# Kernel optimization log

Hardware: AMD Instinct MI355X
Metric: run time of the kernel (lower is better)

Reference implementation:

```python
import jax, jax.numpy as jnp
import numpy as np

SIZE = (4096, 4096)   # self.size
SIGMA = 1.0           # blur_sigma
NOISE_STD = 0.01      # noise_std


def _gauss_kernel(sigma):
    # scipy.ndimage.gaussian_filter: radius = int(truncate*sigma + 0.5), truncate=4.0
    r = int(4.0 * sigma + 0.5)
    x = np.arange(-r, r + 1, dtype=np.float32)
    k = np.exp(-0.5 * (x / sigma) ** 2)
    k = k / k.sum()
    return jnp.asarray(k), r


def _blur(img, sigma):
    # img: [C, H, W]; separable Gaussian, scipy mode='reflect' == jnp symmetric pad
    k, r = _gauss_kernel(sigma)
    x = jnp.pad(img, ((0, 0), (r, r), (r, r)), mode='symmetric')
    x = x[:, None]  # [C, 1, H+2r, W+2r] (NCHW)
    kh = k.reshape(1, 1, -1, 1)
    kw = k.reshape(1, 1, 1, -1)
    x = jax.lax.conv_general_dilated(x, kh, (1, 1), 'VALID')
    x = jax.lax.conv_general_dilated(x, kw, (1, 1), 'VALID')
    return x[:, 0]  # [C, H, W]


def setup_inputs() -> dict:
    key = jax.random.key(0)
    k1, k2 = jax.random.split(key)
    img = jax.random.normal(k1, (1, 2048, 2048), dtype=jnp.float32)
    noise = jax.random.normal(k2, (1,) + SIZE, dtype=jnp.float32)
    return {"img": img, "noise": noise}


def reference(img, noise):
    # bilinear resize, align_corners=False == jax half-pixel linear resize
    img = jax.image.resize(img, (img.shape[0],) + SIZE, method='linear')
    img = jnp.flip(img, axis=2)   # horizontal flip
    img = jnp.flip(img, axis=1)   # vertical flip
    img = jnp.rot90(img, k=1, axes=(1, 2))  # rot90, k fixed to 1
    img = img + noise * NOISE_STD
    img = _blur(img, SIGMA)
    img = jnp.log1p(jnp.clip(img, 0.0))  # clamp(min=0) then log1p
    return img
```

## Files before the change

### kernel.cpp

```cpp
#include <hip/hip_runtime.h>
#include <math.h>

#define N      4096
#define NIMG   2048
#define TXO    56
#define HR     40
#define DRS    48
#define IPP    27
#define IPR    34
#define VB     64
#define NSX    74
#define NSY    103
#define NSTRIP (NSX * NSY)
#define NBLK   ((NSTRIP + 3) / 4)

#define KW0 0.00013383063f
#define KW1 0.00443186160f
#define KW2 0.05399112800f
#define KW3 0.24197144000f
#define KW4 0.39894346870f

__device__ __forceinline__ int symi(int g) {
    g = (g < 0) ? (-1 - g) : g;
    g = (g >= N) ? (2 * N - 1 - g) : g;
    return g;
}

__global__ __launch_bounds__(256, 5)
void TensorAugment_79216376807666_kernel(const float* __restrict__ img,
                                         const float* __restrict__ noise,
                                         float* __restrict__ out) {
    __shared__ float SH[4 * (IPR * IPP + 8 * VB)];

    const int tid  = threadIdx.x;
    const int lane = tid & 63;
    const int wave = tid >> 6;

    float* const IP   = SH + wave * (IPR * IPP + 8 * VB);
    float* const VBUF = IP + IPR * IPP;

    const int strip0 = blockIdx.x * 4 + wave;
    if (strip0 >= NSTRIP) return;

    const int strip = __builtin_amdgcn_readfirstlane(strip0);
    const int sx = strip % NSX;
    const int sy = strip / NSX;
    const int x0 = sx * TXO;
    const int y0 = sy * HR;

    int gxa = x0 - 4, gxb = x0 + 59;
    int mxa = symi(gxa), mxb = symi(gxb);
    int gxmin = min(mxa, mxb), gxmax = max(mxa, mxb);
    if (gxa <= 0) gxmin = 0;
    if (gxb >= N - 1) gxmax = N - 1;
    int umin = (N - 1) - gxmax, umax = (N - 1) - gxmin;
    int r0min = (umin - 1) >> 1;
    int r0max = (umax - 1) >> 1;
    int nrows = r0max - r0min + 2;

    int gya = y0 - 4, gyb = y0 + DRS - 5;
    int mya = symi(gya), myb = symi(gyb);
    int gymin = min(mya, myb), gymax = max(mya, myb);
    if (gya <= 0) gymin = 0;
    if (gyb >= N - 1) gymax = N - 1;
    int c0min = (gymin - 1) >> 1;
    int c0max = (gymax - 1) >> 1;
    int ncols = c0max - c0min + 2;

    {
        const int c  = lane & 31;
        const int rb = lane >> 5;
        const bool cok = (c < ncols);
#pragma unroll
        for (int k = 0; k < 17; ++k) {
            const int r = rb + 2 * k;
            if (cok && r < nrows) {
                const int ir = min(max(r0min + r, 0), NIMG - 1);
                const int ic = min(max(c0min + c, 0), NIMG - 1);
                IP[r * IPP + c] = img[ir * NIMG + ic];
            }
        }
    }

    const int gx  = x0 - 4 + lane;
    const int gxm = symi(gx);
    const int u   = (N - 1) - gxm;
    const int r0  = (u - 1) >> 1;
    const float wr1 = (u & 1) ? 0.25f : 0.75f;
    const float wr0 = 1.0f - wr1;
    const int a0  = (r0 - r0min) * IPP;
    const bool oklane = (lane >= 4) && (lane < 60) && (gx < N);
    const int rbase = min(max(lane - 4, 0), VB - 9);

    const float kk[9] = {KW0, KW1, KW2, KW3, KW4, KW3, KW2, KW1, KW0};

    auto nzld = [&](int dr) -> float {
        const int gym = symi(y0 - 4 + dr);
        return noise[(size_t)gym * N + gxm];
    };
    auto drow = [&](int dr, float nz) -> float {
        const int gym = symi(y0 - 4 + dr);
        const int jc  = ((gym - 1) >> 1) - c0min;
        const float wc1 = (gym & 1) ? 0.25f : 0.75f;
        const float wc0 = 1.0f - wc1;
        const float f0 = IP[a0 + jc],       f1 = IP[a0 + jc + 1];
        const float f2 = IP[a0 + IPP + jc], f3 = IP[a0 + IPP + jc + 1];
        const float top = fmaf(wc0, f0, wc1 * f1);
        const float bot = fmaf(wc0, f2, wc1 * f3);
        return fmaf(0.01f, nz, fmaf(wr0, top, wr1 * bot));
    };

    float win[16];
    {
        float nz[16];
#pragma unroll
        for (int j = 0; j < 16; ++j) nz[j] = nzld(j);
#pragma unroll
        for (int j = 0; j < 16; ++j) win[j] = drow(j, nz[j]);
    }

#pragma unroll 1
    for (int ck = 2; ck <= 6; ++ck) {
        float nz[8];
        if (ck < 6) {
#pragma unroll
            for (int j = 0; j < 8; ++j) nz[j] = nzld(8 * ck + j);
        }

#pragma unroll
        for (int j = 0; j < 8; ++j) {
            float acc = kk[0] * win[j];
#pragma unroll
            for (int i = 1; i < 9; ++i) acc = fmaf(kk[i], win[j + i], acc);
            VBUF[j * VB + lane] = acc;
        }

        const int gyb0 = y0 + 8 * (ck - 2);
#pragma unroll
        for (int j = 0; j < 8; ++j) {
            const int vb = j * VB + rbase;
            float acc = kk[0] * VBUF[vb];
#pragma unroll
            for (int i = 1; i < 9; ++i) acc = fmaf(kk[i], VBUF[vb + i], acc);
            acc = fmaxf(acc, 0.0f);
            const float r = __logf(1.0f + acc);
            const int gy = gyb0 + j;
            if (oklane && gy < N) out[(size_t)gy * N + gx] = r;
        }

        if (ck < 6) {
#pragma unroll
            for (int i = 0; i < 8; ++i) win[i] = win[i + 8];
#pragma unroll
            for (int j = 0; j < 8; ++j) win[8 + j] = drow(8 * ck + j, nz[j]);
        }
    }
}

extern "C" void kernel_launch(void* const* d_in, const int* in_sizes, int n_in,
                              void* d_out, int out_size, void* d_ws, size_t ws_size,
                              hipStream_t stream) {
    const float* img   = (const float*)d_in[0];
    const float* noise = (const float*)d_in[1];
    float* out = (float*)d_out;

    dim3 grid(NBLK);
    TensorAugment_79216376807666_kernel<<<grid, 256, 0, stream>>>(img, noise, out);
}
```

Measured before the change: 149.0 us.

## Replace LDS horizontal blur with ds_bpermute and specialize interior strip upsampling

The horizontal 9-tap pass now exchanges neighbour values across lanes with ds_bpermute instead of writing to and reading back from a shared-memory buffer, which removes the VBUF allocation. The smaller LDS footprint lets launch bounds rise to 6 waves per SIMD. Interior strips also get a fast path that reuses six row-interpolated values to produce eight output rows and loads noise with plain strided addressing instead of per-row reflect arithmetic. The cost is more code, the risk of register pressure under the tighter launch bound, and bpermute latency, which is still LDS-bound.

```diff
diff --git a/kernel.cpp b/kernel.cpp
--- a/kernel.cpp
+++ b/kernel.cpp
@@ -8,7 +8,6 @@
 #define DRS    48
 #define IPP    27
 #define IPR    34
-#define VB     64
 #define NSX    74
 #define NSY    103
 #define NSTRIP (NSX * NSY)
@@ -26,18 +25,54 @@
     return g;
 }
 
-__global__ __launch_bounds__(256, 5)
+
+#define PRODUCE8(M, OFS, NZA, NOFS)                                            \
+    do {                                                                       \
+        if (yin) {                                                             \
+            const int ab_ = a0 + 4 * (M);                                      \
+            float g0 = fmaf(wr0, IP[ab_ + 0], wr1 * IP[ab_ + IPP + 0]);        \
+            float g1 = fmaf(wr0, IP[ab_ + 1], wr1 * IP[ab_ + IPP + 1]);        \
+            float g2 = fmaf(wr0, IP[ab_ + 2], wr1 * IP[ab_ + IPP + 2]);        \
+            float g3 = fmaf(wr0, IP[ab_ + 3], wr1 * IP[ab_ + IPP + 3]);        \
+            float g4 = fmaf(wr0, IP[ab_ + 4], wr1 * IP[ab_ + IPP + 4]);        \
+            float g5 = fmaf(wr0, IP[ab_ + 5], wr1 * IP[ab_ + IPP + 5]);        \
+            win[(OFS) + 0] = fmaf(0.25f, g0, fmaf(0.75f, g1, 0.01f * (NZA)[(NOFS) + 0])); \
+            win[(OFS) + 1] = fmaf(0.75f, g1, fmaf(0.25f, g2, 0.01f * (NZA)[(NOFS) + 1])); \
+            win[(OFS) + 2] = fmaf(0.25f, g1, fmaf(0.75f, g2, 0.01f * (NZA)[(NOFS) + 2])); \
+            win[(OFS) + 3] = fmaf(0.75f, g2, fmaf(0.25f, g3, 0.01f * (NZA)[(NOFS) + 3])); \
+            win[(OFS) + 4] = fmaf(0.25f, g2, fmaf(0.75f, g3, 0.01f * (NZA)[(NOFS) + 4])); \
+            win[(OFS) + 5] = fmaf(0.75f, g3, fmaf(0.25f, g4, 0.01f * (NZA)[(NOFS) + 5])); \
+            win[(OFS) + 6] = fmaf(0.25f, g3, fmaf(0.75f, g4, 0.01f * (NZA)[(NOFS) + 6])); \
+            win[(OFS) + 7] = fmaf(0.75f, g4, fmaf(0.25f, g5, 0.01f * (NZA)[(NOFS) + 7])); \
+        } else {                                                               \
+            _Pragma("unroll")                                                  \
+            for (int j_ = 0; j_ < 8; ++j_) {                                   \
+                const int dr_  = 8 * (M) + j_;                                 \
+                const int gym_ = symi(y0 - 4 + dr_);                           \
+                const int jc_  = ((gym_ - 1) >> 1) - c0min;                    \
+                const float wc1_ = (gym_ & 1) ? 0.25f : 0.75f;                 \
+                const float wc0_ = 1.0f - wc1_;                                \
+                const float f0_ = IP[a0 + jc_],       f1_ = IP[a0 + jc_ + 1];  \
+                const float f2_ = IP[a0 + IPP + jc_], f3_ = IP[a0 + IPP + jc_ + 1]; \
+                const float top_ = fmaf(wc0_, f0_, wc1_ * f1_);                \
+                const float bot_ = fmaf(wc0_, f2_, wc1_ * f3_);                \
+                win[(OFS) + j_] = fmaf(0.01f, (NZA)[(NOFS) + j_],              \
+                                       fmaf(wr0, top_, wr1 * bot_));           \
+            }                                                                  \
+        }                                                                      \
+    } while (0)
+
+__global__ __launch_bounds__(256, 6)
 void TensorAugment_79216376807666_kernel(const float* __restrict__ img,
                                          const float* __restrict__ noise,
                                          float* __restrict__ out) {
-    __shared__ float SH[4 * (IPR * IPP + 8 * VB)];
+    __shared__ float SH[4 * IPR * IPP];
 
     const int tid  = threadIdx.x;
     const int lane = tid & 63;
     const int wave = tid >> 6;
 
-    float* const IP   = SH + wave * (IPR * IPP + 8 * VB);
-    float* const VBUF = IP + IPR * IPP;
+    float* const IP = SH + wave * (IPR * IPP);
 
     const int strip0 = blockIdx.x * 4 + wave;
     if (strip0 >= NSTRIP) return;
@@ -47,6 +82,7 @@
     const int sy = strip / NSX;
     const int x0 = sx * TXO;
     const int y0 = sy * HR;
+    const bool yin = (sy > 0) && (sy < NSY - 1);
 
     int gxa = x0 - 4, gxb = x0 + 59;
     int mxa = symi(gxa), mxb = symi(gxb);
@@ -90,58 +126,65 @@
     const float wr0 = 1.0f - wr1;
     const int a0  = (r0 - r0min) * IPP;
     const bool oklane = (lane >= 4) && (lane < 60) && (gx < N);
-    const int rbase = min(max(lane - 4, 0), VB - 9);
-
-    const float kk[9] = {KW0, KW1, KW2, KW3, KW4, KW3, KW2, KW1, KW0};
-
-    auto nzld = [&](int dr) -> float {
-        const int gym = symi(y0 - 4 + dr);
-        return noise[(size_t)gym * N + gxm];
-    };
-    auto drow = [&](int dr, float nz) -> float {
-        const int gym = symi(y0 - 4 + dr);
-        const int jc  = ((gym - 1) >> 1) - c0min;
-        const float wc1 = (gym & 1) ? 0.25f : 0.75f;
-        const float wc0 = 1.0f - wc1;
-        const float f0 = IP[a0 + jc],       f1 = IP[a0 + jc + 1];
-        const float f2 = IP[a0 + IPP + jc], f3 = IP[a0 + IPP + jc + 1];
-        const float top = fmaf(wc0, f0, wc1 * f1);
-        const float bot = fmaf(wc0, f2, wc1 * f3);
-        return fmaf(0.01f, nz, fmaf(wr0, top, wr1 * bot));
-    };
+
+    int ba[9];
+#pragma unroll
+    for (int d = 0; d < 9; ++d) ba[d] = 4 * (lane + d - 4);
+
+    const float* const nzb = noise + ((size_t)max(y0 - 4, 0) * N + gxm);
 
     float win[16];
     {
-        float nz[16];
-#pragma unroll
-        for (int j = 0; j < 16; ++j) nz[j] = nzld(j);
-#pragma unroll
-        for (int j = 0; j < 16; ++j) win[j] = drow(j, nz[j]);
+        float nzp[16];
+        if (yin) {
+#pragma unroll
+            for (int j = 0; j < 16; ++j) nzp[j] = nzb[(size_t)j * N];
+        } else {
+#pragma unroll
+            for (int j = 0; j < 16; ++j)
+                nzp[j] = noise[(size_t)symi(y0 - 4 + j) * N + gxm];
+        }
+        PRODUCE8(0, 0, nzp, 0);
+        PRODUCE8(1, 8, nzp, 8);
     }
 
 #pragma unroll 1
     for (int ck = 2; ck <= 6; ++ck) {
-        float nz[8];
+        float nz8[8];
         if (ck < 6) {
-#pragma unroll
-            for (int j = 0; j < 8; ++j) nz[j] = nzld(8 * ck + j);
-        }
-
+            if (yin) {
+                const float* nr = nzb + (size_t)(8 * ck) * N;
+#pragma unroll
+                for (int j = 0; j < 8; ++j) nz8[j] = nr[(size_t)j * N];
+            } else {
+#pragma unroll
+                for (int j = 0; j < 8; ++j)
+                    nz8[j] = noise[(size_t)symi(y0 - 4 + 8 * ck + j) * N + gxm];
+            }
+        }
+
+        const int gyb0 = y0 + 8 * (ck - 2);
 #pragma unroll
         for (int j = 0; j < 8; ++j) {
-            float acc = kk[0] * win[j];
-#pragma unroll
-            for (int i = 1; i < 9; ++i) acc = fmaf(kk[i], win[j + i], acc);
-            VBUF[j * VB + lane] = acc;
-        }
-
-        const int gyb0 = y0 + 8 * (ck - 2);
-#pragma unroll
-        for (int j = 0; j < 8; ++j) {
-            const int vb = j * VB + rbase;
-            float acc = kk[0] * VBUF[vb];
-#pragma unroll
-            for (int i = 1; i < 9; ++i) acc = fmaf(kk[i], VBUF[vb + i], acc);
+            float v = KW0 * win[j];
+            v = fmaf(KW1, win[j + 1], v);
+            v = fmaf(KW2, win[j + 2], v);
+            v = fmaf(KW3, win[j + 3], v);
+            v = fmaf(KW4, win[j + 4], v);
+            v = fmaf(KW3, win[j + 5], v);
+            v = fmaf(KW2, win[j + 6], v);
+            v = fmaf(KW1, win[j + 7], v);
+            v = fmaf(KW0, win[j + 8], v);
+            const int vi = __float_as_int(v);
+            float acc = KW4 * v;
+            acc = fmaf(KW0, __int_as_float(__builtin_amdgcn_ds_bpermute(ba[0], vi)), acc);
+            acc = fmaf(KW1, __int_as_float(__builtin_amdgcn_ds_bpermute(ba[1], vi)), acc);
+            acc = fmaf(KW2, __int_as_float(__builtin_amdgcn_ds_bpermute(ba[2], vi)), acc);
+            acc = fmaf(KW3, __int_as_float(__builtin_amdgcn_ds_bpermute(ba[3], vi)), acc);
+            acc = fmaf(KW3, __int_as_float(__builtin_amdgcn_ds_bpermute(ba[5], vi)), acc);
+            acc = fmaf(KW2, __int_as_float(__builtin_amdgcn_ds_bpermute(ba[6], vi)), acc);
+            acc = fmaf(KW1, __int_as_float(__builtin_amdgcn_ds_bpermute(ba[7], vi)), acc);
+            acc = fmaf(KW0, __int_as_float(__builtin_amdgcn_ds_bpermute(ba[8], vi)), acc);
             acc = fmaxf(acc, 0.0f);
             const float r = __logf(1.0f + acc);
             const int gy = gyb0 + j;
@@ -151,8 +194,7 @@
         if (ck < 6) {
 #pragma unroll
             for (int i = 0; i < 8; ++i) win[i] = win[i + 8];
-#pragma unroll
-            for (int j = 0; j < 8; ++j) win[8 + j] = drow(8 * ck + j, nz[j]);
+            PRODUCE8(ck, 8, nz8, 0);
         }
     }
 }
```

New measurement: 145.9 us. -2.1%, faster.

## Widen strips to 4 columns per lane with float4 I/O and interior fast path

Applied to the files above, without the earlier changes.

Each wave now covers a 256-wide by 16-row strip, with every lane producing 4 adjacent output columns through float4 noise loads and float4 stores. Interior strips take a specialized path that computes the bilinear upsample with fixed 0.25/0.75 weights and no reflection index math, while border strips keep a general path. The horizontal pass exchanges neighbor quads through a small double-buffered LDS slot instead of a 64-wide row buffer. The aim is less scalar memory traffic, less index arithmetic and less halo overhead. In exchange it uses more registers per thread, lowers the occupancy hint from 5 to 4, and spends more of each strip on vertical halo rows.

```diff
diff --git a/kernel.cpp b/kernel.cpp
--- a/kernel.cpp
+++ b/kernel.cpp
@@ -3,14 +3,16 @@
 
 #define N      4096
 #define NIMG   2048
-#define TXO    56
-#define HR     40
-#define DRS    48
-#define IPP    27
-#define IPR    34
-#define VB     64
-#define NSX    74
-#define NSY    103
+#define SPAN   256
+#define TXN    248
+#define HR     16
+#define DRS    24
+#define IPP    15
+#define IPR    130
+#define IPOFF  1952
+#define WSZ    (IPOFF + 512)
+#define NSX    17
+#define NSY    256
 #define NSTRIP (NSX * NSY)
 #define NBLK   ((NSTRIP + 3) / 4)
 
@@ -26,18 +28,82 @@
     return g;
 }
 
-__global__ __launch_bounds__(256, 5)
+#define H9(A,B,C,D,E,F,G,H,I)                                                  \
+    fmaf(KW0,(A), fmaf(KW1,(B), fmaf(KW2,(C), fmaf(KW3,(D), fmaf(KW4,(E),     \
+    fmaf(KW3,(F), fmaf(KW2,(G), fmaf(KW1,(H), KW0*(I)))))))))
+
+#define GCOL(J, G) do {                                                        \
+    const float p0_ = IP[ipb - 2*IPP + (J)];                                   \
+    const float p1_ = IP[ipb -   IPP + (J)];                                   \
+    const float p2_ = IP[ipb         + (J)];                                   \
+    const float p3_ = IP[ipb +   IPP + (J)];                                   \
+    (G).x = fmaf(0.75f, p2_, 0.25f * p3_);                                     \
+    (G).y = fmaf(0.25f, p1_, 0.75f * p2_);                                     \
+    (G).z = fmaf(0.75f, p1_, 0.25f * p2_);                                     \
+    (G).w = fmaf(0.25f, p0_, 0.75f * p1_);                                     \
+} while (0)
+
+#define DMIX(DST, W0, GA_, W1, GB_, NZ) do {                                   \
+    (DST).x = fmaf(W0, (GA_).x, fmaf(W1, (GB_).x, 0.01f * (NZ).x));            \
+    (DST).y = fmaf(W0, (GA_).y, fmaf(W1, (GB_).y, 0.01f * (NZ).y));            \
+    (DST).z = fmaf(W0, (GA_).z, fmaf(W1, (GB_).z, 0.01f * (NZ).z));            \
+    (DST).w = fmaf(W0, (GA_).w, fmaf(W1, (GB_).w, 0.01f * (NZ).w));            \
+} while (0)
+
+#define PROD4F(JN, W0_, W1_, W2_, W3_, Z0, Z1, Z2, Z3) do {                    \
+    float4 gc_, gd_;                                                           \
+    GCOL((JN), gc_);  GCOL((JN) + 1, gd_);                                     \
+    DMIX(W0_, 0.25f, ga, 0.75f, gb,  Z0);                                      \
+    DMIX(W1_, 0.75f, gb, 0.25f, gc_, Z1);                                      \
+    DMIX(W2_, 0.25f, gb, 0.75f, gc_, Z2);                                      \
+    DMIX(W3_, 0.75f, gc_, 0.25f, gd_, Z3);                                     \
+    ga = gc_;  gb = gd_;                                                       \
+} while (0)
+
+#define OUT1(K, GY) do {                                                       \
+    float4 v_;                                                                 \
+    v_.x = H9(win[K].x, win[K+1].x, win[K+2].x, win[K+3].x, win[K+4].x,        \
+              win[K+5].x, win[K+6].x, win[K+7].x, win[K+8].x);                 \
+    v_.y = H9(win[K].y, win[K+1].y, win[K+2].y, win[K+3].y, win[K+4].y,        \
+              win[K+5].y, win[K+6].y, win[K+7].y, win[K+8].y);                 \
+    v_.z = H9(win[K].z, win[K+1].z, win[K+2].z, win[K+3].z, win[K+4].z,        \
+              win[K+5].z, win[K+6].z, win[K+7].z, win[K+8].z);                 \
+    v_.w = H9(win[K].w, win[K+1].w, win[K+2].w, win[K+3].w, win[K+4].w,        \
+              win[K+5].w, win[K+6].w, win[K+7].w, win[K+8].w);                 \
+    float* vx_ = ((K) & 1) ? VX1 : VX0;                                        \
+    *reinterpret_cast<float4*>(vx_ + 4 * lane) = v_;                           \
+    const float4 wl_ = *reinterpret_cast<const float4*>(vx_ + 4 * lnL);        \
+    const float4 wr_ = *reinterpret_cast<const float4*>(vx_ + 4 * lnR);        \
+    float4 r_;                                                                 \
+    r_.x = H9(wl_.x, wl_.y, wl_.z, wl_.w, v_.x, v_.y, v_.z, v_.w, wr_.x);      \
+    r_.y = H9(wl_.y, wl_.z, wl_.w, v_.x, v_.y, v_.z, v_.w, wr_.x, wr_.y);      \
+    r_.z = H9(wl_.z, wl_.w, v_.x, v_.y, v_.z, v_.w, wr_.x, wr_.y, wr_.z);      \
+    r_.w = H9(wl_.w, v_.x, v_.y, v_.z, v_.w, wr_.x, wr_.y, wr_.z, wr_.w);      \
+    r_.x = __logf(1.0f + fmaxf(r_.x, 0.0f));                                   \
+    r_.y = __logf(1.0f + fmaxf(r_.y, 0.0f));                                   \
+    r_.z = __logf(1.0f + fmaxf(r_.z, 0.0f));                                   \
+    r_.w = __logf(1.0f + fmaxf(r_.w, 0.0f));                                   \
+    if (okst) *reinterpret_cast<float4*>(out + (size_t)(GY) * N + gxs) = r_;   \
+} while (0)
+
+#define SLIDE4() do {                                                          \
+    _Pragma("unroll")                                                          \
+    for (int i_ = 0; i_ < 8; ++i_) win[i_] = win[i_ + 4];                      \
+} while (0)
+
+__global__ __launch_bounds__(256, 4)
 void TensorAugment_79216376807666_kernel(const float* __restrict__ img,
                                          const float* __restrict__ noise,
                                          float* __restrict__ out) {
-    __shared__ float SH[4 * (IPR * IPP + 8 * VB)];
+    __shared__ __align__(16) float SH[4 * WSZ];
 
     const int tid  = threadIdx.x;
     const int lane = tid & 63;
     const int wave = tid >> 6;
 
-    float* const IP   = SH + wave * (IPR * IPP + 8 * VB);
-    float* const VBUF = IP + IPR * IPP;
+    float* const IP  = SH + wave * WSZ;
+    float* const VX0 = IP + IPOFF;
+    float* const VX1 = VX0 + 256;
 
     const int strip0 = blockIdx.x * 4 + wave;
     if (strip0 >= NSTRIP) return;
@@ -45,10 +111,12 @@
     const int strip = __builtin_amdgcn_readfirstlane(strip0);
     const int sx = strip % NSX;
     const int sy = strip / NSX;
-    const int x0 = sx * TXO;
+    const int x0 = sx * TXN;
     const int y0 = sy * HR;
-
-    int gxa = x0 - 4, gxb = x0 + 59;
+    const bool xin = (sx > 0) && (sx < NSX - 1);
+    const bool yin = (sy > 0) && (sy < NSY - 1);
+
+    int gxa = x0 - 4, gxb = x0 + SPAN - 5;
     int mxa = symi(gxa), mxb = symi(gxb);
     int gxmin = min(mxa, mxb), gxmax = max(mxa, mxb);
     if (gxa <= 0) gxmin = 0;
@@ -68,12 +136,12 @@
     int ncols = c0max - c0min + 2;
 
     {
-        const int c  = lane & 31;
-        const int rb = lane >> 5;
+        const int c  = lane & 15;
+        const int rb = lane >> 4;
         const bool cok = (c < ncols);
 #pragma unroll
-        for (int k = 0; k < 17; ++k) {
-            const int r = rb + 2 * k;
+        for (int k = 0; k < 33; ++k) {
+            const int r = rb + 4 * k;
             if (cok && r < nrows) {
                 const int ir = min(max(r0min + r, 0), NIMG - 1);
                 const int ic = min(max(c0min + c, 0), NIMG - 1);
@@ -82,77 +150,117 @@
         }
     }
 
-    const int gx  = x0 - 4 + lane;
-    const int gxm = symi(gx);
-    const int u   = (N - 1) - gxm;
-    const int r0  = (u - 1) >> 1;
-    const float wr1 = (u & 1) ? 0.25f : 0.75f;
-    const float wr0 = 1.0f - wr1;
-    const int a0  = (r0 - r0min) * IPP;
-    const bool oklane = (lane >= 4) && (lane < 60) && (gx < N);
-    const int rbase = min(max(lane - 4, 0), VB - 9);
-
-    const float kk[9] = {KW0, KW1, KW2, KW3, KW4, KW3, KW2, KW1, KW0};
-
-    auto nzld = [&](int dr) -> float {
-        const int gym = symi(y0 - 4 + dr);
-        return noise[(size_t)gym * N + gxm];
-    };
-    auto drow = [&](int dr, float nz) -> float {
-        const int gym = symi(y0 - 4 + dr);
-        const int jc  = ((gym - 1) >> 1) - c0min;
-        const float wc1 = (gym & 1) ? 0.25f : 0.75f;
-        const float wc0 = 1.0f - wc1;
-        const float f0 = IP[a0 + jc],       f1 = IP[a0 + jc + 1];
-        const float f2 = IP[a0 + IPP + jc], f3 = IP[a0 + IPP + jc + 1];
-        const float top = fmaf(wc0, f0, wc1 * f1);
-        const float bot = fmaf(wc0, f2, wc1 * f3);
-        return fmaf(0.01f, nz, fmaf(wr0, top, wr1 * bot));
-    };
-
-    float win[16];
-    {
-        float nz[16];
+    const int gxs  = x0 - 4 + 4 * lane;
+    const bool okst = (lane >= 1) && (lane <= 62) && (gxs <= N - 4);
+    const int lnL = (lane == 0) ? 0 : lane - 1;
+    const int lnR = (lane == 63) ? 63 : lane + 1;
+
+    if (xin && yin) {
+        const int m   = 2049 - (x0 >> 1) - 2 * lane;
+        const int ipb = (m - r0min) * IPP;
+        const float* const nzb = noise + ((size_t)(y0 - 4) * N + gxs);
+#define LDNZ(DR) (*reinterpret_cast<const float4*>(nzb + (size_t)(DR) * N))
+
+        float4 win[12];
+        float4 ga, gb;
+        GCOL(0, ga);
+        GCOL(1, gb);
+
+        {
+            float4 n0 = LDNZ(0), n1 = LDNZ(1), n2 = LDNZ(2), n3 = LDNZ(3);
+            float4 n4 = LDNZ(4), n5 = LDNZ(5), n6 = LDNZ(6), n7 = LDNZ(7);
+            PROD4F(2, win[0], win[1], win[2], win[3], n0, n1, n2, n3);
+            float4 n8 = LDNZ(8), n9 = LDNZ(9), na = LDNZ(10), nb = LDNZ(11);
+            PROD4F(4, win[4], win[5], win[6], win[7], n4, n5, n6, n7);
+            PROD4F(6, win[8], win[9], win[10], win[11], n8, n9, na, nb);
+        }
+        {
+            float4 n0 = LDNZ(12), n1 = LDNZ(13), n2 = LDNZ(14), n3 = LDNZ(15);
+            OUT1(0, y0 + 0);  OUT1(1, y0 + 1);  OUT1(2, y0 + 2);  OUT1(3, y0 + 3);
+            SLIDE4();
+            PROD4F(8, win[8], win[9], win[10], win[11], n0, n1, n2, n3);
+        }
+        {
+            float4 n0 = LDNZ(16), n1 = LDNZ(17), n2 = LDNZ(18), n3 = LDNZ(19);
+            OUT1(0, y0 + 4);  OUT1(1, y0 + 5);  OUT1(2, y0 + 6);  OUT1(3, y0 + 7);
+            SLIDE4();
+            PROD4F(10, win[8], win[9], win[10], win[11], n0, n1, n2, n3);
+        }
+        {
+            float4 n0 = LDNZ(20), n1 = LDNZ(21), n2 = LDNZ(22), n3 = LDNZ(23);
+            OUT1(0, y0 + 8);  OUT1(1, y0 + 9);  OUT1(2, y0 + 10); OUT1(3, y0 + 11);
+            SLIDE4();
+            PROD4F(12, win[8], win[9], win[10], win[11], n0, n1, n2, n3);
+        }
+        OUT1(0, y0 + 12); OUT1(1, y0 + 13); OUT1(2, y0 + 14); OUT1(3, y0 + 15);
+#undef LDNZ
+    } else {
+        const int gxm0 = symi(gxs + 0), gxm1 = symi(gxs + 1);
+        const int gxm2 = symi(gxs + 2), gxm3 = symi(gxs + 3);
+        const int u0 = (N - 1) - gxm0, u1 = (N - 1) - gxm1;
+        const int u2 = (N - 1) - gxm2, u3 = (N - 1) - gxm3;
+        const int A0 = (((u0 - 1) >> 1) - r0min) * IPP;
+        const int A1 = (((u1 - 1) >> 1) - r0min) * IPP;
+        const int A2 = (((u2 - 1) >> 1) - r0min) * IPP;
+        const int A3 = (((u3 - 1) >> 1) - r0min) * IPP;
+        const float w10 = (u0 & 1) ? 0.25f : 0.75f, w00 = 1.0f - w10;
+        const float w11 = (u1 & 1) ? 0.25f : 0.75f, w01 = 1.0f - w11;
+        const float w12 = (u2 & 1) ? 0.25f : 0.75f, w02 = 1.0f - w12;
+        const float w13 = (u3 & 1) ? 0.25f : 0.75f, w03 = 1.0f - w13;
+
+        auto nzg = [&](int dr) -> float4 {
+            const float* nr = noise + (size_t)symi(y0 - 4 + dr) * N;
+            float4 r;
+            r.x = nr[gxm0]; r.y = nr[gxm1]; r.z = nr[gxm2]; r.w = nr[gxm3];
+            return r;
+        };
+        auto dgen = [&](int dr, float4 nz) -> float4 {
+            const int gym = symi(y0 - 4 + dr);
+            const int jc  = ((gym - 1) >> 1) - c0min;
+            const float wc1 = (gym & 1) ? 0.25f : 0.75f;
+            const float wc0 = 1.0f - wc1;
+            float4 r;
+            {
+                const float t = fmaf(wc0, IP[A0 + jc], wc1 * IP[A0 + jc + 1]);
+                const float b = fmaf(wc0, IP[A0 + IPP + jc], wc1 * IP[A0 + IPP + jc + 1]);
+                r.x = fmaf(w00, t, fmaf(w10, b, 0.01f * nz.x));
+            }
+            {
+                const float t = fmaf(wc0, IP[A1 + jc], wc1 * IP[A1 + jc + 1]);
+                const float b = fmaf(wc0, IP[A1 + IPP + jc], wc1 * IP[A1 + IPP + jc + 1]);
+                r.y = fmaf(w01, t, fmaf(w11, b, 0.01f * nz.y));
+            }
+            {
+                const float t = fmaf(wc0, IP[A2 + jc], wc1 * IP[A2 + jc + 1]);
+                const float b = fmaf(wc0, IP[A2 + IPP + jc], wc1 * IP[A2 + IPP + jc + 1]);
+                r.z = fmaf(w02, t, fmaf(w12, b, 0.01f * nz.z));
+            }
+            {
+                const float t = fmaf(wc0, IP[A3 + jc], wc1 * IP[A3 + jc + 1]);
+                const float b = fmaf(wc0, IP[A3 + IPP + jc], wc1 * IP[A3 + IPP + jc + 1]);
+                r.w = fmaf(w03, t, fmaf(w13, b, 0.01f * nz.w));
+            }
+            return r;
+        };
+
+        float4 win[12];
 #pragma unroll
-        for (int j = 0; j < 16; ++j) nz[j] = nzld(j);
+        for (int j = 0; j < 12; ++j) win[j] = dgen(j, nzg(j));
+
 #pragma unroll
-        for (int j = 0; j < 16; ++j) win[j] = drow(j, nz[j]);
-    }
-
-#pragma unroll 1
-    for (int ck = 2; ck <= 6; ++ck) {
-        float nz[8];
-        if (ck < 6) {
-#pragma unroll
-            for (int j = 0; j < 8; ++j) nz[j] = nzld(8 * ck + j);
-        }
-
-#pragma unroll
-        for (int j = 0; j < 8; ++j) {
-            float acc = kk[0] * win[j];
-#pragma unroll
-            for (int i = 1; i < 9; ++i) acc = fmaf(kk[i], win[j + i], acc);
-            VBUF[j * VB + lane] = acc;
-        }
-
-        const int gyb0 = y0 + 8 * (ck - 2);
-#pragma unroll
-        for (int j = 0; j < 8; ++j) {
-            const int vb = j * VB + rbase;
-            float acc = kk[0] * VBUF[vb];
-#pragma unroll
-            for (int i = 1; i < 9; ++i) acc = fmaf(kk[i], VBUF[vb + i], acc);
-            acc = fmaxf(acc, 0.0f);
-            const float r = __logf(1.0f + acc);
-            const int gy = gyb0 + j;
-            if (oklane && gy < N) out[(size_t)gy * N + gx] = r;
-        }
-
-        if (ck < 6) {
-#pragma unroll
-            for (int i = 0; i < 8; ++i) win[i] = win[i + 8];
-#pragma unroll
-            for (int j = 0; j < 8; ++j) win[8 + j] = drow(8 * ck + j, nz[j]);
+        for (int c = 0; c < 4; ++c) {
+            float4 n0, n1, n2, n3;
+            if (c < 3) { n0 = nzg(12 + 4*c); n1 = nzg(13 + 4*c);
+                         n2 = nzg(14 + 4*c); n3 = nzg(15 + 4*c); }
+            OUT1(0, y0 + 4*c + 0);  OUT1(1, y0 + 4*c + 1);
+            OUT1(2, y0 + 4*c + 2);  OUT1(3, y0 + 4*c + 3);
+            if (c < 3) {
+                SLIDE4();
+                win[8]  = dgen(12 + 4*c, n0);
+                win[9]  = dgen(13 + 4*c, n1);
+                win[10] = dgen(14 + 4*c, n2);
+                win[11] = dgen(15 + 4*c, n3);
+            }
         }
     }
 }
```

Result: slower. 194.3 us (+30.4%).

## Restructure blur to 2-px-per-lane tiles with shared block image patch

Applied to the files above, without the earlier changes.

Each lane now produces two adjacent output columns using float2 noise loads and stores, with the four waves sharing one 120x64 block tile and a single cooperatively loaded image patch behind a __syncthreads. Interior tiles take a fast path with no reflection math that reuses bilinear column interpolations across consecutive rows, while border tiles keep the general symmetric-index path. The horizontal pass exchanges values through small per-wave LDS buffers instead of a full 8-row buffer. The aim is to cut redundant halo loads, LDS traffic and per-element index arithmetic, at the cost of more registers, a block barrier and a duplicated code path.

```diff
diff --git a/kernel.cpp b/kernel.cpp
--- a/kernel.cpp
+++ b/kernel.cpp
@@ -3,16 +3,14 @@
 
 #define N      4096
 #define NIMG   2048
-#define TXO    56
-#define HR     40
-#define DRS    48
-#define IPP    27
-#define IPR    34
-#define VB     64
-#define NSX    74
-#define NSY    103
-#define NSTRIP (NSX * NSY)
-#define NBLK   ((NSTRIP + 3) / 4)
+#define SPAN   128
+#define TXN    120
+#define HRW    16
+#define PP     66
+#define PR     66
+#define NSX    35
+#define NSY    64
+#define NBLK   (NSX * NSY)
 
 #define KW0 0.00013383063f
 #define KW1 0.00443186160f
@@ -26,29 +24,86 @@
     return g;
 }
 
+#define H9(A,B,C,D,E,F,G,H,I)                                                  \
+    fmaf(KW0,(A), fmaf(KW1,(B), fmaf(KW2,(C), fmaf(KW3,(D), fmaf(KW4,(E),      \
+    fmaf(KW3,(F), fmaf(KW2,(G), fmaf(KW1,(H), KW0*(I)))))))))
+
+#define GCOL2(J, G) do {                                                       \
+    const float p0_ = ipg[(J) - PP];                                           \
+    const float p1_ = ipg[(J)];                                                \
+    const float p2_ = ipg[(J) + PP];                                           \
+    (G).x = fmaf(0.75f, p1_, 0.25f * p2_);                                     \
+    (G).y = fmaf(0.25f, p0_, 0.75f * p1_);                                     \
+} while (0)
+
+#define PROD4(J2, D0, D1, D2, D3, Z0, Z1, Z2, Z3) do {                         \
+    float2 gc_, gd_;                                                           \
+    GCOL2((J2), gc_); GCOL2((J2) + 1, gd_);                                    \
+    (D0).x = fmaf(0.25f, ga.x, fmaf(0.75f, gb.x, 0.01f * (Z0).x));             \
+    (D0).y = fmaf(0.25f, ga.y, fmaf(0.75f, gb.y, 0.01f * (Z0).y));             \
+    (D1).x = fmaf(0.75f, gb.x, fmaf(0.25f, gc_.x, 0.01f * (Z1).x));            \
+    (D1).y = fmaf(0.75f, gb.y, fmaf(0.25f, gc_.y, 0.01f * (Z1).y));            \
+    (D2).x = fmaf(0.25f, gb.x, fmaf(0.75f, gc_.x, 0.01f * (Z2).x));            \
+    (D2).y = fmaf(0.25f, gb.y, fmaf(0.75f, gc_.y, 0.01f * (Z2).y));            \
+    (D3).x = fmaf(0.75f, gc_.x, fmaf(0.25f, gd_.x, 0.01f * (Z3).x));           \
+    (D3).y = fmaf(0.75f, gc_.y, fmaf(0.25f, gd_.y, 0.01f * (Z3).y));           \
+    ga = gc_; gb = gd_;                                                        \
+} while (0)
+
+#define OUT1(K, GY) do {                                                       \
+    float2 v_;                                                                 \
+    v_.x = H9(win[K].x, win[K+1].x, win[K+2].x, win[K+3].x, win[K+4].x,        \
+              win[K+5].x, win[K+6].x, win[K+7].x, win[K+8].x);                 \
+    v_.y = H9(win[K].y, win[K+1].y, win[K+2].y, win[K+3].y, win[K+4].y,        \
+              win[K+5].y, win[K+6].y, win[K+7].y, win[K+8].y);                 \
+    float* sl_ = ((K) & 1) ? EX1 : EX0;                                        \
+    *reinterpret_cast<float2*>(sl_ + 2 * lane) = v_;                           \
+    const float2 l0_ = *reinterpret_cast<const float2*>(sl_ + oL0);            \
+    const float2 l1_ = *reinterpret_cast<const float2*>(sl_ + oL1);            \
+    const float2 r0_ = *reinterpret_cast<const float2*>(sl_ + oR0);            \
+    const float2 r1_ = *reinterpret_cast<const float2*>(sl_ + oR1);            \
+    float ox_ = KW0 * l0_.x; ox_ = fmaf(KW1, l0_.y, ox_);                      \
+    ox_ = fmaf(KW2, l1_.x, ox_); ox_ = fmaf(KW3, l1_.y, ox_);                  \
+    ox_ = fmaf(KW4, v_.x, ox_);  ox_ = fmaf(KW3, v_.y, ox_);                   \
+    ox_ = fmaf(KW2, r0_.x, ox_); ox_ = fmaf(KW1, r0_.y, ox_);                  \
+    ox_ = fmaf(KW0, r1_.x, ox_);                                               \
+    float oy_ = KW0 * l0_.y; oy_ = fmaf(KW1, l1_.x, oy_);                      \
+    oy_ = fmaf(KW2, l1_.y, oy_); oy_ = fmaf(KW3, v_.x, oy_);                   \
+    oy_ = fmaf(KW4, v_.y, oy_);  oy_ = fmaf(KW3, r0_.x, oy_);                  \
+    oy_ = fmaf(KW2, r0_.y, oy_); oy_ = fmaf(KW1, r1_.x, oy_);                  \
+    oy_ = fmaf(KW0, r1_.y, oy_);                                               \
+    float2 rr_;                                                                \
+    rr_.x = __logf(1.0f + fmaxf(ox_, 0.0f));                                   \
+    rr_.y = __logf(1.0f + fmaxf(oy_, 0.0f));                                   \
+    if (okst) *reinterpret_cast<float2*>(out + (size_t)(GY) * N + gxs) = rr_;  \
+} while (0)
+
+#define SLIDE4() do {                                                          \
+    _Pragma("unroll")                                                          \
+    for (int i_ = 0; i_ < 8; ++i_) win[i_] = win[i_ + 4];                      \
+} while (0)
+
 __global__ __launch_bounds__(256, 5)
 void TensorAugment_79216376807666_kernel(const float* __restrict__ img,
                                          const float* __restrict__ noise,
                                          float* __restrict__ out) {
-    __shared__ float SH[4 * (IPR * IPP + 8 * VB)];
+    __shared__ __align__(16) float SH[PR * PP + 4 * 256];
 
     const int tid  = threadIdx.x;
     const int lane = tid & 63;
     const int wave = tid >> 6;
 
-    float* const IP   = SH + wave * (IPR * IPP + 8 * VB);
-    float* const VBUF = IP + IPR * IPP;
-
-    const int strip0 = blockIdx.x * 4 + wave;
-    if (strip0 >= NSTRIP) return;
-
-    const int strip = __builtin_amdgcn_readfirstlane(strip0);
-    const int sx = strip % NSX;
-    const int sy = strip / NSX;
-    const int x0 = sx * TXO;
-    const int y0 = sy * HR;
-
-    int gxa = x0 - 4, gxb = x0 + 59;
+    float* const IP  = SH;
+    float* const EX0 = SH + PR * PP + wave * 256;
+    float* const EX1 = EX0 + 128;
+
+    const int bid = blockIdx.x;
+    const int sx  = bid % NSX;
+    const int sy  = bid / NSX;
+    const int x0  = sx * TXN;
+    const int y0  = sy * 64;
+
+    int gxa = x0 - 4, gxb = x0 + SPAN - 5;
     int mxa = symi(gxa), mxb = symi(gxb);
     int gxmin = min(mxa, mxb), gxmax = max(mxa, mxb);
     if (gxa <= 0) gxmin = 0;
@@ -58,101 +113,120 @@
     int r0max = (umax - 1) >> 1;
     int nrows = r0max - r0min + 2;
 
-    int gya = y0 - 4, gyb = y0 + DRS - 5;
+    int gya = y0 - 4, gyb = y0 + 67;
     int mya = symi(gya), myb = symi(gyb);
     int gymin = min(mya, myb), gymax = max(mya, myb);
     if (gya <= 0) gymin = 0;
     if (gyb >= N - 1) gymax = N - 1;
     int c0min = (gymin - 1) >> 1;
-    int c0max = (gymax - 1) >> 1;
-    int ncols = c0max - c0min + 2;
 
     {
-        const int c  = lane & 31;
-        const int rb = lane >> 5;
-        const bool cok = (c < ncols);
+        const int gcol = min(max(c0min + lane, 0), NIMG - 1);
+        for (int r = wave; r < nrows; r += 4) {
+            const int ir = min(max(r0min + r, 0), NIMG - 1);
+            IP[r * PP + lane] = img[ir * NIMG + gcol];
+        }
+    }
+    __syncthreads();
+
+    const int y0w = y0 + HRW * wave;
+    const int gxs = x0 - 4 + 2 * lane;
+    const bool okst = (lane >= 2) && (lane <= 61) && (gxs <= N - 2);
+    const bool yin  = (y0w >= 4) && (y0w + 19 <= N - 1);
+    const bool xin  = (sx > 0) && (sx < NSX - 1);
+    const int oL0 = max(2 * lane - 4, 0), oL1 = max(2 * lane - 2, 0);
+    const int oR0 = min(2 * lane + 2, 126), oR1 = min(2 * lane + 4, 126);
+
+    float2 win[12];
+
+    if (xin && yin) {
+        const int a    = (x0 >> 1) - 2 + lane;
+        const int ipb  = (2047 - a - r0min) * PP;
+        const float* const ipg = IP + ipb;
+        const int jb   = ((y0w - 5) >> 1) - c0min;
+        const float* const nzb = noise + ((size_t)(y0w - 4) * N + gxs);
+#define LDNZ(DR) (*reinterpret_cast<const float2*>(nzb + (size_t)(DR) * N))
+
+        float2 ga, gb;
+        GCOL2(jb, ga);
+        GCOL2(jb + 1, gb);
+
+        {
+            float2 n0 = LDNZ(0), n1 = LDNZ(1), n2 = LDNZ(2),  n3 = LDNZ(3);
+            float2 n4 = LDNZ(4), n5 = LDNZ(5), n6 = LDNZ(6),  n7 = LDNZ(7);
+            float2 n8 = LDNZ(8), n9 = LDNZ(9), na = LDNZ(10), nb = LDNZ(11);
+            PROD4(jb + 2, win[0], win[1], win[2],  win[3],  n0, n1, n2, n3);
+            PROD4(jb + 4, win[4], win[5], win[6],  win[7],  n4, n5, n6, n7);
+            PROD4(jb + 6, win[8], win[9], win[10], win[11], n8, n9, na, nb);
+        }
+        {
+            float2 n0 = LDNZ(12), n1 = LDNZ(13), n2 = LDNZ(14), n3 = LDNZ(15);
+            OUT1(0, y0w + 0); OUT1(1, y0w + 1); OUT1(2, y0w + 2); OUT1(3, y0w + 3);
+            SLIDE4();
+            PROD4(jb + 8, win[8], win[9], win[10], win[11], n0, n1, n2, n3);
+        }
+        {
+            float2 n0 = LDNZ(16), n1 = LDNZ(17), n2 = LDNZ(18), n3 = LDNZ(19);
+            OUT1(0, y0w + 4); OUT1(1, y0w + 5); OUT1(2, y0w + 6); OUT1(3, y0w + 7);
+            SLIDE4();
+            PROD4(jb + 10, win[8], win[9], win[10], win[11], n0, n1, n2, n3);
+        }
+        {
+            float2 n0 = LDNZ(20), n1 = LDNZ(21), n2 = LDNZ(22), n3 = LDNZ(23);
+            OUT1(0, y0w + 8); OUT1(1, y0w + 9); OUT1(2, y0w + 10); OUT1(3, y0w + 11);
+            SLIDE4();
+            PROD4(jb + 12, win[8], win[9], win[10], win[11], n0, n1, n2, n3);
+        }
+        OUT1(0, y0w + 12); OUT1(1, y0w + 13); OUT1(2, y0w + 14); OUT1(3, y0w + 15);
+#undef LDNZ
+    } else {
+        const int gxm0 = symi(gxs), gxm1 = symi(gxs + 1);
+        const int u0 = (N - 1) - gxm0, u1 = (N - 1) - gxm1;
+        const int A0 = (((u0 - 1) >> 1) - r0min) * PP;
+        const int A1 = (((u1 - 1) >> 1) - r0min) * PP;
+        const float w10 = (u0 & 1) ? 0.25f : 0.75f, w00 = 1.0f - w10;
+        const float w11 = (u1 & 1) ? 0.25f : 0.75f, w01 = 1.0f - w11;
+
+        auto nzg = [&](int dr) -> float2 {
+            const float* nr = noise + (size_t)symi(y0w - 4 + dr) * N;
+            float2 r; r.x = nr[gxm0]; r.y = nr[gxm1]; return r;
+        };
+        auto dgen = [&](int dr, float2 nz) -> float2 {
+            const int gym = symi(y0w - 4 + dr);
+            const int jc  = ((gym - 1) >> 1) - c0min;
+            const float wc1 = (gym & 1) ? 0.25f : 0.75f;
+            const float wc0 = 1.0f - wc1;
+            float2 r;
+            {
+                const float t = fmaf(wc0, IP[A0 + jc], wc1 * IP[A0 + jc + 1]);
+                const float b = fmaf(wc0, IP[A0 + PP + jc], wc1 * IP[A0 + PP + jc + 1]);
+                r.x = fmaf(w00, t, fmaf(w10, b, 0.01f * nz.x));
+            }
+            {
+                const float t = fmaf(wc0, IP[A1 + jc], wc1 * IP[A1 + jc + 1]);
+                const float b = fmaf(wc0, IP[A1 + PP + jc], wc1 * IP[A1 + PP + jc + 1]);
+                r.y = fmaf(w01, t, fmaf(w11, b, 0.01f * nz.y));
+            }
+            return r;
+        };
+
 #pragma unroll
-        for (int k = 0; k < 17; ++k) {
-            const int r = rb + 2 * k;
-            if (cok && r < nrows) {
-                const int ir = min(max(r0min + r, 0), NIMG - 1);
-                const int ic = min(max(c0min + c, 0), NIMG - 1);
-                IP[r * IPP + c] = img[ir * NIMG + ic];
+        for (int j = 0; j < 12; ++j) win[j] = dgen(j, nzg(j));
+
+#pragma unroll
+        for (int c = 0; c < 4; ++c) {
+            float2 n0, n1, n2, n3;
+            if (c < 3) { n0 = nzg(12 + 4 * c); n1 = nzg(13 + 4 * c);
+                         n2 = nzg(14 + 4 * c); n3 = nzg(15 + 4 * c); }
+            OUT1(0, y0w + 4 * c + 0); OUT1(1, y0w + 4 * c + 1);
+            OUT1(2, y0w + 4 * c + 2); OUT1(3, y0w + 4 * c + 3);
+            if (c < 3) {
+                SLIDE4();
+                win[8]  = dgen(12 + 4 * c, n0);
+                win[9]  = dgen(13 + 4 * c, n1);
+                win[10] = dgen(14 + 4 * c, n2);
+                win[11] = dgen(15 + 4 * c, n3);
             }
-        }
-    }
-
-    const int gx  = x0 - 4 + lane;
-    const int gxm = symi(gx);
-    const int u   = (N - 1) - gxm;
-    const int r0  = (u - 1) >> 1;
-    const float wr1 = (u & 1) ? 0.25f : 0.75f;
-    const float wr0 = 1.0f - wr1;
-    const int a0  = (r0 - r0min) * IPP;
-    const bool oklane = (lane >= 4) && (lane < 60) && (gx < N);
-    const int rbase = min(max(lane - 4, 0), VB - 9);
-
-    const float kk[9] = {KW0, KW1, KW2, KW3, KW4, KW3, KW2, KW1, KW0};
-
-    auto nzld = [&](int dr) -> float {
-        const int gym = symi(y0 - 4 + dr);
-        return noise[(size_t)gym * N + gxm];
-    };
-    auto drow = [&](int dr, float nz) -> float {
-        const int gym = symi(y0 - 4 + dr);
-        const int jc  = ((gym - 1) >> 1) - c0min;
-        const float wc1 = (gym & 1) ? 0.25f : 0.75f;
-        const float wc0 = 1.0f - wc1;
-        const float f0 = IP[a0 + jc],       f1 = IP[a0 + jc + 1];
-        const float f2 = IP[a0 + IPP + jc], f3 = IP[a0 + IPP + jc + 1];
-        const float top = fmaf(wc0, f0, wc1 * f1);
-        const float bot = fmaf(wc0, f2, wc1 * f3);
-        return fmaf(0.01f, nz, fmaf(wr0, top, wr1 * bot));
-    };
-
-    float win[16];
-    {
-        float nz[16];
-#pragma unroll
-        for (int j = 0; j < 16; ++j) nz[j] = nzld(j);
-#pragma unroll
-        for (int j = 0; j < 16; ++j) win[j] = drow(j, nz[j]);
-    }
-
-#pragma unroll 1
-    for (int ck = 2; ck <= 6; ++ck) {
-        float nz[8];
-        if (ck < 6) {
-#pragma unroll
-            for (int j = 0; j < 8; ++j) nz[j] = nzld(8 * ck + j);
-        }
-
-#pragma unroll
-        for (int j = 0; j < 8; ++j) {
-            float acc = kk[0] * win[j];
-#pragma unroll
-            for (int i = 1; i < 9; ++i) acc = fmaf(kk[i], win[j + i], acc);
-            VBUF[j * VB + lane] = acc;
-        }
-
-        const int gyb0 = y0 + 8 * (ck - 2);
-#pragma unroll
-        for (int j = 0; j < 8; ++j) {
-            const int vb = j * VB + rbase;
-            float acc = kk[0] * VBUF[vb];
-#pragma unroll
-            for (int i = 1; i < 9; ++i) acc = fmaf(kk[i], VBUF[vb + i], acc);
-            acc = fmaxf(acc, 0.0f);
-            const float r = __logf(1.0f + acc);
-            const int gy = gyb0 + j;
-            if (oklane && gy < N) out[(size_t)gy * N + gx] = r;
-        }
-
-        if (ck < 6) {
-#pragma unroll
-            for (int i = 0; i < 8; ++i) win[i] = win[i + 8];
-#pragma unroll
-            for (int j = 0; j < 8; ++j) win[8 + j] = drow(8 * ck + j, nz[j]);
         }
     }
 }
```

Result: faster. 140.6 us (-5.7%).
